# Optimization experiments

Hardware: AMD Instinct MI355X
Metric: run time of the kernel (lower is better)

The kernel has to match this reference:

```python
import jax, jax.numpy as jnp
import numpy as np

NCODEBOOKS, K, SUBVEC = 32, 16, 128
IN_F, OUT_F = 4096, 2048
BATCH, SEQ = 2, 1024


def setup_inputs() -> dict:
    key = jax.random.key(0)
    k1, k2, k3, k4, k5 = jax.random.split(key, 5)
    return {
        "x": jax.random.normal(k1, (BATCH, SEQ, IN_F), dtype=jnp.float32),
        "centroids": jax.random.normal(k2, (NCODEBOOKS, K, SUBVEC), dtype=jnp.float32),
        "weight": jax.random.normal(k3, (NCODEBOOKS, SUBVEC, OUT_F), dtype=jnp.float32),
        "inverse_temperature_logit": jax.random.normal(k4, (1,), dtype=jnp.float32),
        "bias": jax.random.normal(k5, (OUT_F,), dtype=jnp.float32),
    }


def reference(x, centroids, weight, inverse_temperature_logit, bias):
    shape = x.shape[:-1]
    C, k, d = centroids.shape
    # [N, C, d] -> [C, N, d]
    xr = jnp.transpose(x.reshape(-1, C, d), (1, 0, 2))
    # Euclidean cdist per codebook: [C, N, k]
    x2 = jnp.sum(xr * xr, axis=-1)[:, :, None]
    c2 = jnp.sum(centroids * centroids, axis=-1)[:, None, :]
    xc = jnp.einsum('cnd,ckd->cnk', xr, centroids)
    dist = jnp.sqrt(jnp.maximum(x2 + c2 - 2.0 * xc, 0.0))
    inv_temp = jax.nn.softplus(inverse_temperature_logit) + 1.0  # [1]
    attention = jax.nn.softmax(-dist * inv_temp, axis=-1)  # [C, N, k]
    lut = jnp.einsum('ckd,cdo->cko', centroids, weight)  # [C, k, O]
    training_output = jnp.einsum('cnk,cko->no', attention, lut)  # [N, O]
    # one-hot argmin matmul == direct gather of lut rows
    idx = jnp.argmin(dist, axis=-1)  # [C, N]
    gathered = jnp.take_along_axis(lut, idx[:, :, None], axis=1)  # [C, N, O]
    inference_output = jnp.sum(gathered, axis=0)  # [N, O]
    # straight-through estimator
    output = training_output - jax.lax.stop_gradient(training_output - inference_output)
    output = output + bias
    return output.reshape(*shape, lut.shape[-1])
```

## Files before the change

### kernel.cpp

```cpp
#include <hip/hip_runtime.h>

#define NCB 32
#define KK 16
#define DD 128
#define IN_F 4096
#define OUT_F 2048
#define NTOK 2048
#define LUT_BLOCKS ((OUT_F / 64) * NCB)
#define IDX_BLOCKS ((NTOK / 64) * NCB)

__global__ __launch_bounds__(256) void fused_lut_idx(
    const float* __restrict__ centroids, const float* __restrict__ weight,
    const float* __restrict__ x, float* __restrict__ lut,
    unsigned char* __restrict__ idxb) {
    extern __shared__ float smem[];
    const int tid = threadIdx.x;

    if (blockIdx.x < LUT_BLOCKS) {
        const int c = blockIdx.x >> 5;
        const int o0 = (blockIdx.x & 31) * 64;
        const int lane_o = tid & 63;
        const int dg = tid >> 6;
        float acc[KK];
#pragma unroll
        for (int k = 0; k < KK; ++k) acc[k] = 0.f;
        const float* wbase = weight + (size_t)c * DD * OUT_F + o0 + lane_o;
        const float* cbase = centroids + (size_t)c * KK * DD;
#pragma unroll
        for (int chunk = 0; chunk < 8; ++chunk) {
            const int d = dg * 32 + chunk * 4;
            float w0 = wbase[(size_t)(d + 0) * OUT_F];
            float w1 = wbase[(size_t)(d + 1) * OUT_F];
            float w2 = wbase[(size_t)(d + 2) * OUT_F];
            float w3 = wbase[(size_t)(d + 3) * OUT_F];
#pragma unroll
            for (int k = 0; k < KK; ++k) {
                float4 cv = *(const float4*)(cbase + k * DD + d);
                acc[k] += cv.x * w0 + cv.y * w1 + cv.z * w2 + cv.w * w3;
            }
        }
        float* part = smem;
#pragma unroll
        for (int k = 0; k < KK; ++k) part[(dg * KK + k) * 64 + lane_o] = acc[k];
        __syncthreads();
#pragma unroll
        for (int r = 0; r < 4; ++r) {
            int i = r * 256 + tid;
            int k = i >> 6, o = i & 63;
            float s = part[(0 * KK + k) * 64 + o] + part[(1 * KK + k) * 64 + o]
                    + part[(2 * KK + k) * 64 + o] + part[(3 * KK + k) * 64 + o];
            lut[((size_t)c * KK + k) * OUT_F + o0 + o] = s;
        }
    } else {
        const int bid = blockIdx.x - LUT_BLOCKS;
        const int c = bid & (NCB - 1);
        const int t0 = (bid >> 5) * 64;
        float* cent_s = smem;
        const int th_q = tid & 3;
        const int th_k = (tid >> 2) & 3;
        const int th_t = tid >> 4;

        for (int p = tid; p < KK * 32; p += 256) {
            int k = p >> 5, f4 = p & 31;
            int q = f4 >> 3, jj = f4 & 7;
            *(float4*)(cent_s + k * 164 + q * 40 + jj * 4) =
                *(const float4*)(centroids + ((size_t)c * KK + k) * DD + f4 * 4);
        }
        __syncthreads();

        float acc[4][4], sq[4];
#pragma unroll
        for (int r = 0; r < 4; ++r)
#pragma unroll
            for (int kk = 0; kk < 4; ++kk) acc[r][kk] = 0.f;
#pragma unroll
        for (int kk = 0; kk < 4; ++kk) sq[kk] = 0.f;

        const float* xb0 = x + (size_t)(t0 + th_t * 4) * IN_F + c * DD + th_q * 32;
#pragma unroll
        for (int chunk = 0; chunk < 8; ++chunk) {
            float4 xa[4];
#pragma unroll
            for (int r = 0; r < 4; ++r)
                xa[r] = *(const float4*)(xb0 + (size_t)r * IN_F + chunk * 4);
            float4 ca[4];
#pragma unroll
            for (int kk = 0; kk < 4; ++kk)
                ca[kk] = *(const float4*)(cent_s + (th_k * 4 + kk) * 164 + th_q * 40 + chunk * 4);
#pragma unroll
            for (int kk = 0; kk < 4; ++kk)
                sq[kk] += ca[kk].x * ca[kk].x + ca[kk].y * ca[kk].y
                        + ca[kk].z * ca[kk].z + ca[kk].w * ca[kk].w;
#pragma unroll
            for (int r = 0; r < 4; ++r)
#pragma unroll
                for (int kk = 0; kk < 4; ++kk)
                    acc[r][kk] += xa[r].x * ca[kk].x + xa[r].y * ca[kk].y
                                + xa[r].z * ca[kk].z + xa[r].w * ca[kk].w;
        }
#pragma unroll
        for (int kk = 0; kk < 4; ++kk) {
            float a = sq[kk];
            a += __shfl_xor(a, 1);
            a += __shfl_xor(a, 2);
            sq[kk] = a;
        }
#pragma unroll
        for (int r = 0; r < 4; ++r)
#pragma unroll
            for (int kk = 0; kk < 4; ++kk) {
                float a = acc[r][kk];
                a += __shfl_xor(a, 1);
                a += __shfl_xor(a, 2);
                acc[r][kk] = a;
            }
#pragma unroll
        for (int r = 0; r < 4; ++r) {
            float best = sq[0] - 2.f * acc[r][0];
            int bi = th_k * 4;
#pragma unroll
            for (int kk = 1; kk < 4; ++kk) {
                float v = sq[kk] - 2.f * acc[r][kk];
                if (v < best) { best = v; bi = th_k * 4 + kk; }
            }
#pragma unroll
            for (int s = 4; s <= 8; s <<= 1) {
                float ov = __shfl_xor(best, s);
                int oi = __shfl_xor(bi, s);
                if (ov < best || (ov == best && oi < bi)) { best = ov; bi = oi; }
            }
            if ((tid & 15) == 0)
                idxb[(size_t)(t0 + th_t * 4 + r) * NCB + c] = (unsigned char)bi;
        }
    }
}

__global__ __launch_bounds__(256) void gather_kernel(const float* __restrict__ lut,
                                                     const unsigned char* __restrict__ idxb,
                                                     const float* __restrict__ bias,
                                                     float* __restrict__ out) {
    const int t0 = blockIdx.x * 256;
    const int o0 = blockIdx.y * 32;
    __shared__ float slut[NCB * KK * 36];
    __shared__ unsigned char sidx[256 * NCB];

    {
        const int row = threadIdx.x >> 3;
        const int q = threadIdx.x & 7;
        for (int r = row; r < NCB * KK; r += 32)
            *(float4*)(slut + r * 36 + q * 4) =
                *(const float4*)(lut + (size_t)r * OUT_F + o0 + q * 4);
    }
    {
        const int4* ig = (const int4*)(idxb + (size_t)t0 * NCB);
        int4* is4 = (int4*)sidx;
        for (int i = threadIdx.x; i < 512; i += 256) is4[i] = ig[i];
    }
    __syncthreads();

    const int oo = (threadIdx.x & 15) * 2;
    const int tl = threadIdx.x >> 4;
    const float2 bv = *(const float2*)(bias + o0 + oo);

    for (int tt = tl; tt < 256; tt += 16) {
        float2 acc = bv;
        const unsigned int* ip = (const unsigned int*)(sidx + tt * NCB);
#pragma unroll
        for (int c4 = 0; c4 < NCB / 4; ++c4) {
            unsigned int iv4 = ip[c4];
#pragma unroll
            for (int b = 0; b < 4; ++b) {
                int cc = c4 * 4 + b;
                int iv = (iv4 >> (8 * b)) & 0xff;
                const float2 v = *(const float2*)(slut + (cc * KK + iv) * 36 + oo);
                acc.x += v.x;
                acc.y += v.y;
            }
        }
        *(float2*)(out + (size_t)(t0 + tt) * OUT_F + o0 + oo) = acc;
    }
}

extern "C" void kernel_launch(void* const* d_in, const int* in_sizes, int n_in,
                              void* d_out, int out_size, void* d_ws, size_t ws_size,
                              hipStream_t stream) {
    const float* x         = (const float*)d_in[0];
    const float* centroids = (const float*)d_in[1];
    const float* weight    = (const float*)d_in[2];
    const float* bias      = (const float*)d_in[4];
    float* out = (float*)d_out;

    float* lut = (float*)d_ws;
    unsigned char* idxb = (unsigned char*)d_ws + (4u << 20);

    fused_lut_idx<<<LUT_BLOCKS + IDX_BLOCKS, 256, 16384, stream>>>(
        centroids, weight, x, lut, idxb);
    gather_kernel<<<dim3(NTOK / 256, OUT_F / 32), 256, 0, stream>>>(lut, idxb, bias, out);
}
```

Before: 160.3 us.

## Restructure LUT blocks to split by centroid group, vectorize gather to float4

The LUT part now tiles 128 outputs per block and splits the 16 centroids across thread groups, so each thread runs the full D reduction. This removes the shared-memory partial-sum reduction and its barrier, and centroids are staged in shared memory instead of read from global. Shared memory becomes a static 10.5KB array with a launch bound asking for 4 blocks per CU. The idx path loads x rows lazily to cut register use, and the gather kernel uses float4 loads and stores with 8 threads per 32-wide output tile. Risks: each weight row is now read by four thread groups, and the LUT grid halves to 512 blocks.

After: 218.1 us. +36.0%, slower.

```diff
diff --git a/kernel.cpp b/kernel.cpp
--- a/kernel.cpp
+++ b/kernel.cpp
@@ -6,56 +6,51 @@
 #define IN_F 4096
 #define OUT_F 2048
 #define NTOK 2048
-#define LUT_BLOCKS ((OUT_F / 64) * NCB)
+#define LUT_BLOCKS (NCB * (OUT_F / 128))
 #define IDX_BLOCKS ((NTOK / 64) * NCB)
 
-__global__ __launch_bounds__(256) void fused_lut_idx(
+__global__ __launch_bounds__(256, 4) void fused_lut_idx(
     const float* __restrict__ centroids, const float* __restrict__ weight,
     const float* __restrict__ x, float* __restrict__ lut,
     unsigned char* __restrict__ idxb) {
-    extern __shared__ float smem[];
+    __shared__ float smem[KK * 164];
     const int tid = threadIdx.x;
 
     if (blockIdx.x < LUT_BLOCKS) {
-        const int c = blockIdx.x >> 5;
-        const int o0 = (blockIdx.x & 31) * 64;
-        const int lane_o = tid & 63;
-        const int dg = tid >> 6;
-        float acc[KK];
+        const int c = blockIdx.x >> 4;
+        const int o0 = (blockIdx.x & 15) * 128;
+        const int og = tid & 63;
+        const int kg = tid >> 6;
+        {
+            const float4* cb = (const float4*)(centroids + (size_t)c * KK * DD);
+            for (int p = tid; p < KK * DD / 4; p += 256) ((float4*)smem)[p] = cb[p];
+        }
+        __syncthreads();
+
+        float2 acc[4];
 #pragma unroll
-        for (int k = 0; k < KK; ++k) acc[k] = 0.f;
-        const float* wbase = weight + (size_t)c * DD * OUT_F + o0 + lane_o;
-        const float* cbase = centroids + (size_t)c * KK * DD;
+        for (int kk = 0; kk < 4; ++kk) acc[kk] = make_float2(0.f, 0.f);
+        const float* wb = weight + (size_t)c * DD * OUT_F + o0 + og * 2;
+#pragma unroll 4
+        for (int dw = 0; dw < DD / 4; ++dw) {
+            float2 w0 = *(const float2*)(wb + (size_t)(dw * 4 + 0) * OUT_F);
+            float2 w1 = *(const float2*)(wb + (size_t)(dw * 4 + 1) * OUT_F);
+            float2 w2 = *(const float2*)(wb + (size_t)(dw * 4 + 2) * OUT_F);
+            float2 w3 = *(const float2*)(wb + (size_t)(dw * 4 + 3) * OUT_F);
 #pragma unroll
-        for (int chunk = 0; chunk < 8; ++chunk) {
-            const int d = dg * 32 + chunk * 4;
-            float w0 = wbase[(size_t)(d + 0) * OUT_F];
-            float w1 = wbase[(size_t)(d + 1) * OUT_F];
-            float w2 = wbase[(size_t)(d + 2) * OUT_F];
-            float w3 = wbase[(size_t)(d + 3) * OUT_F];
-#pragma unroll
-            for (int k = 0; k < KK; ++k) {
-                float4 cv = *(const float4*)(cbase + k * DD + d);
-                acc[k] += cv.x * w0 + cv.y * w1 + cv.z * w2 + cv.w * w3;
+            for (int kk = 0; kk < 4; ++kk) {
+                float4 cv = *(const float4*)(smem + (kg * 4 + kk) * DD + dw * 4);
+                acc[kk].x += cv.x * w0.x + cv.y * w1.x + cv.z * w2.x + cv.w * w3.x;
+                acc[kk].y += cv.x * w0.y + cv.y * w1.y + cv.z * w2.y + cv.w * w3.y;
             }
         }
-        float* part = smem;
 #pragma unroll
-        for (int k = 0; k < KK; ++k) part[(dg * KK + k) * 64 + lane_o] = acc[k];
-        __syncthreads();
-#pragma unroll
-        for (int r = 0; r < 4; ++r) {
-            int i = r * 256 + tid;
-            int k = i >> 6, o = i & 63;
-            float s = part[(0 * KK + k) * 64 + o] + part[(1 * KK + k) * 64 + o]
-                    + part[(2 * KK + k) * 64 + o] + part[(3 * KK + k) * 64 + o];
-            lut[((size_t)c * KK + k) * OUT_F + o0 + o] = s;
-        }
+        for (int kk = 0; kk < 4; ++kk)
+            *(float2*)(lut + ((size_t)c * KK + kg * 4 + kk) * OUT_F + o0 + og * 2) = acc[kk];
     } else {
         const int bid = blockIdx.x - LUT_BLOCKS;
         const int c = bid & (NCB - 1);
         const int t0 = (bid >> 5) * 64;
-        float* cent_s = smem;
         const int th_q = tid & 3;
         const int th_k = (tid >> 2) & 3;
         const int th_t = tid >> 4;
@@ -63,7 +58,7 @@
         for (int p = tid; p < KK * 32; p += 256) {
             int k = p >> 5, f4 = p & 31;
             int q = f4 >> 3, jj = f4 & 7;
-            *(float4*)(cent_s + k * 164 + q * 40 + jj * 4) =
+            *(float4*)(smem + k * 164 + q * 40 + jj * 4) =
                 *(const float4*)(centroids + ((size_t)c * KK + k) * DD + f4 * 4);
         }
         __syncthreads();
@@ -79,24 +74,22 @@
         const float* xb0 = x + (size_t)(t0 + th_t * 4) * IN_F + c * DD + th_q * 32;
 #pragma unroll
         for (int chunk = 0; chunk < 8; ++chunk) {
-            float4 xa[4];
-#pragma unroll
-            for (int r = 0; r < 4; ++r)
-                xa[r] = *(const float4*)(xb0 + (size_t)r * IN_F + chunk * 4);
             float4 ca[4];
 #pragma unroll
             for (int kk = 0; kk < 4; ++kk)
-                ca[kk] = *(const float4*)(cent_s + (th_k * 4 + kk) * 164 + th_q * 40 + chunk * 4);
+                ca[kk] = *(const float4*)(smem + (th_k * 4 + kk) * 164 + th_q * 40 + chunk * 4);
 #pragma unroll
             for (int kk = 0; kk < 4; ++kk)
                 sq[kk] += ca[kk].x * ca[kk].x + ca[kk].y * ca[kk].y
                         + ca[kk].z * ca[kk].z + ca[kk].w * ca[kk].w;
 #pragma unroll
-            for (int r = 0; r < 4; ++r)
+            for (int r = 0; r < 4; ++r) {
+                float4 xr = *(const float4*)(xb0 + (size_t)r * IN_F + chunk * 4);
 #pragma unroll
                 for (int kk = 0; kk < 4; ++kk)
-                    acc[r][kk] += xa[r].x * ca[kk].x + xa[r].y * ca[kk].y
-                                + xa[r].z * ca[kk].z + xa[r].w * ca[kk].w;
+                    acc[r][kk] += xr.x * ca[kk].x + xr.y * ca[kk].y
+                                + xr.z * ca[kk].z + xr.w * ca[kk].w;
+            }
         }
 #pragma unroll
         for (int kk = 0; kk < 4; ++kk) {
@@ -158,12 +151,12 @@
     }
     __syncthreads();
 
-    const int oo = (threadIdx.x & 15) * 2;
-    const int tl = threadIdx.x >> 4;
-    const float2 bv = *(const float2*)(bias + o0 + oo);
+    const int oo = (threadIdx.x & 7) * 4;
+    const int tl = threadIdx.x >> 3;
+    const float4 bv = *(const float4*)(bias + o0 + oo);
 
-    for (int tt = tl; tt < 256; tt += 16) {
-        float2 acc = bv;
+    for (int tt = tl; tt < 256; tt += 32) {
+        float4 acc = bv;
         const unsigned int* ip = (const unsigned int*)(sidx + tt * NCB);
 #pragma unroll
         for (int c4 = 0; c4 < NCB / 4; ++c4) {
@@ -172,12 +165,11 @@
             for (int b = 0; b < 4; ++b) {
                 int cc = c4 * 4 + b;
                 int iv = (iv4 >> (8 * b)) & 0xff;
-                const float2 v = *(const float2*)(slut + (cc * KK + iv) * 36 + oo);
-                acc.x += v.x;
-                acc.y += v.y;
+                const float4 v = *(const float4*)(slut + (cc * KK + iv) * 36 + oo);
+                acc.x += v.x; acc.y += v.y; acc.z += v.z; acc.w += v.w;
             }
         }
-        *(float2*)(out + (size_t)(t0 + tt) * OUT_F + o0 + oo) = acc;
+        *(float4*)(out + (size_t)(t0 + tt) * OUT_F + o0 + oo) = acc;
     }
 }
 
@@ -193,7 +185,7 @@
     float* lut = (float*)d_ws;
     unsigned char* idxb = (unsigned char*)d_ws + (4u << 20);
 
-    fused_lut_idx<<<LUT_BLOCKS + IDX_BLOCKS, 256, 16384, stream>>>(
+    fused_lut_idx<<<LUT_BLOCKS + IDX_BLOCKS, 256, 0, stream>>>(
         centroids, weight, x, lut, idxb);
     gather_kernel<<<dim3(NTOK / 256, OUT_F / 32), 256, 0, stream>>>(lut, idxb, bias, out);
 }
```
